# Optimization experiments

Measured on AMD Instinct MI355X. Metric: run time of the kernel, lower is better.

## Reference

```python
import jax, jax.numpy as jnp
import numpy as np

IH, IW = 32, 32
HEADS = 8
DIM_HEAD = 64
SCALE = DIM_HEAD ** -0.5


def _make_relative_index():
    # Matches torch buffer: ceil Euclidean distance between all pairs of 2D coords.
    ii, jj = np.meshgrid(np.arange(IH), np.arange(IW), indexing='ij')
    coords = np.stack([ii.ravel(), jj.ravel()])  # [2, n]
    rel = coords[:, :, None] - coords[:, None, :]  # [2, n, n]
    dist = np.ceil(np.sqrt(rel[0] ** 2 + rel[1] ** 2))
    return jnp.asarray(dist.astype(np.int32).ravel())  # [n*n]


def setup_inputs() -> dict:
    key = jax.random.key(0)
    k1, k2, k3, k4 = jax.random.split(key, 4)
    b, n, inp = 32, IH * IW, 512
    inner = HEADS * DIM_HEAD
    diag = int(np.ceil(np.sqrt((IH - 1) ** 2 + (IW - 1) ** 2)))
    return {
        'x': jax.random.normal(k1, (b, n, inp), jnp.float32),
        'w_qkv': jax.random.normal(k2, (inp, inner * 3), jnp.float32) * (inp ** -0.5),
        'bias_table': jax.random.normal(k3, (diag + 1, HEADS), jnp.float32) * 0.02,
        'w_out': jax.random.normal(k4, (inner, 512), jnp.float32) * (inner ** -0.5),
        'b_out': jnp.zeros((512,), jnp.float32),
        'relative_index': _make_relative_index(),
    }


def reference(x, w_qkv, bias_table, w_out, b_out, relative_index):
    b, n, _ = x.shape
    qkv = x @ w_qkv  # [b, n, 3*inner]
    q, k, v = jnp.split(qkv, 3, axis=-1)
    def to_heads(t):
        return t.reshape(b, n, HEADS, DIM_HEAD).transpose(0, 2, 1, 3)  # b h n d
    q, k, v = to_heads(q), to_heads(k), to_heads(v)
    dots = jnp.einsum('bhid,bhjd->bhij', q, k) * SCALE  # [b, h, n, n]
    # gather relative bias: [n*n, h] -> [1, h, n, n]
    rel_bias = bias_table[relative_index].reshape(n, n, HEADS).transpose(2, 0, 1)
    attn = jax.nn.softmax(dots + rel_bias[None], axis=-1)
    out = jnp.einsum('bhij,bhjd->bhid', attn, v)  # b h n d
    out = out.transpose(0, 2, 1, 3).reshape(b, n, HEADS * DIM_HEAD)
    return out @ w_out + b_out
```

## Files before the change

kernel.cpp:

```cpp
#include <hip/hip_runtime.h>
#include <hip/hip_bf16.h>
#include <cstdint>

typedef __bf16 bf16_t;
typedef bf16_t bf16x8 __attribute__((ext_vector_type(8)));
typedef float f32x4 __attribute__((ext_vector_type(4)));
typedef float f32x16 __attribute__((ext_vector_type(16)));
typedef unsigned u32x4 __attribute__((ext_vector_type(4)));

#define MFMA16(a, b, c) __builtin_amdgcn_mfma_f32_16x16x32_bf16(a, b, c, 0, 0, 0)
#define MFMA32(a, b, c) __builtin_amdgcn_mfma_f32_32x32x16_bf16(a, b, c, 0, 0, 0)

#define GLOAD_LDS16(g, l)                                                  \
    __builtin_amdgcn_global_load_lds(                                      \
        (const __attribute__((address_space(1))) unsigned*)(g),            \
        (__attribute__((address_space(3))) unsigned*)(l), 16, 0, 0)

constexpr int LDK = 72;

#define QSCALE 0.1803368801f
#define LOG2E 1.44269504f

__global__ void zero_out(unsigned short* __restrict__ out, long n) {
    long i = (long)blockIdx.x * 256 + threadIdx.x;
    if (i < n) out[i] = 0;
}

__global__ void detect_dtype(const unsigned* __restrict__ x,
                             int* __restrict__ flag) {
    if (threadIdx.x == 0 && blockIdx.x == 0) {
        int cnt = 0;
        for (int i = 0; i < 1024; ++i) {
            unsigned e = (x[i] >> 7) & 0xFF;
            cnt += (e > 100 && e < 150) ? 1 : 0;
        }
        *flag = (cnt > 512) ? 1 : 0;
    }
}

__global__ __launch_bounds__(256) void convert_x(const void* __restrict__ in,
                                                 bf16_t* __restrict__ out,
                                                 const int* __restrict__ flagp) {
    const int fl = *flagp;
    long i = ((long)blockIdx.x * 256 + threadIdx.x) * 8;
    if (fl) {
        *(bf16x8*)&out[i] = *(const bf16x8*)&((const bf16_t*)in)[i];
    } else {
        f32x4 lo = *(const f32x4*)&((const float*)in)[i];
        f32x4 hi = *(const f32x4*)&((const float*)in)[i + 4];
        bf16x8 v;
#pragma unroll
        for (int e = 0; e < 4; ++e) {
            v[e] = (bf16_t)lo[e];
            v[e + 4] = (bf16_t)hi[e];
        }
        *(bf16x8*)&out[i] = v;
    }
}

__global__ void transpose_flex(const void* __restrict__ in,
                               bf16_t* __restrict__ out, int R, int C,
                               const int* __restrict__ flagp, int scale_rows) {
    const int fl = *flagp;
    __shared__ bf16_t tile[32][33];
    int c0 = blockIdx.x * 32, r0 = blockIdx.y * 32;
    int x = threadIdx.x, y = threadIdx.y;
#pragma unroll
    for (int i = 0; i < 4; ++i) {
        long idx = (long)(r0 + y + 8 * i) * C + c0 + x;
        float fv = fl ? (float)((const bf16_t*)in)[idx]
                      : ((const float*)in)[idx];
        if (c0 + x < scale_rows) fv *= QSCALE;
        tile[y + 8 * i][x] = (bf16_t)fv;
    }
    __syncthreads();
#pragma unroll
    for (int i = 0; i < 4; ++i)
        out[(long)(c0 + y + 8 * i) * R + r0 + x] = tile[x][y + 8 * i];
}

__global__ __launch_bounds__(256) void build_bias_perm(
    const int* __restrict__ rel_index, const void* __restrict__ bias_table,
    float* __restrict__ perm, const int* __restrict__ flagp) {
    const int fl = *flagp;
    const int jt = blockIdx.x;
    const int qb = blockIdx.y;
    const int t = threadIdx.x;
    const int lane = t & 63;
    const int h = (t >> 6) + 4 * blockIdx.z;
    const int i = qb * 32 + (lane & 31);
    const int hi = lane >> 5;
    float out[16];
#pragma unroll
    for (int r = 0; r < 16; ++r) {
        int j = jt * 32 + (r & 3) + 8 * (r >> 2) + 4 * hi;
        int ridx = rel_index[i * 1024 + j];
        ridx = ridx < 0 ? 0 : (ridx > 44 ? 44 : ridx);
        float bv = fl ? (float)((const bf16_t*)bias_table)[ridx * 8 + h]
                      : ((const float*)bias_table)[ridx * 8 + h];
        out[r] = bv * LOG2E;
    }
    long off = (((long)(h * 32 + qb) * 32 + jt) << 10) + lane * 16;
#pragma unroll
    for (int g = 0; g < 4; ++g)
        *(f32x4*)&perm[off + 4 * g] = *(f32x4*)&out[4 * g];
}

__global__ __launch_bounds__(256) void transpose_v(
    const bf16_t* __restrict__ qkv, bf16_t* __restrict__ vt) {
    __shared__ bf16_t tile[64 * 64];
    const int jt = blockIdx.x;
    const int bh = blockIdx.y;
    const int b = bh >> 3, h = bh & 7;
    const bf16_t* src = qkv + (long)b * 1024 * 1536 + 1024 + h * 64;
    const int t = threadIdx.x;
    const int r = t >> 3, c8 = t & 7;
    const int j0 = jt * 64;
#pragma unroll
    for (int rep = 0; rep < 2; ++rep) {
        int jj = r + 32 * rep;
        *(bf16x8*)&tile[jj * 64 + ((c8 ^ (jj >> 3)) << 3)] =
            *(const bf16x8*)&src[(long)(j0 + jj) * 1536 + c8 * 8];
    }
    __syncthreads();
#pragma unroll
    for (int rep = 0; rep < 2; ++rep) {
        int dd = r + 32 * rep;
        int jc = c8 * 8;
        bf16_t o[8];
#pragma unroll
        for (int e = 0; e < 8; ++e) {
            int row = jc + e;
            o[e] = tile[row * 64 + (((dd >> 3) ^ (row >> 3)) << 3) + (dd & 7)];
        }
        *(bf16x8*)&vt[((long)bh << 16) + (long)dd * 1024 + j0 + jc] =
            *(bf16x8*)&o[0];
    }
}

template <bool BIAS, bool OUTFLEX>
__global__ __launch_bounds__(256) void gemm_lds(
    const bf16_t* __restrict__ A, const bf16_t* __restrict__ Bt, int K,
    int lda, long a_row0, void* __restrict__ C, int ldc, long c_row0,
    const void* __restrict__ bias, const int* __restrict__ flagp) {
    const int fl = *flagp;
    __shared__ bf16_t a_lds[128 * 64];
    __shared__ bf16_t b_lds[128 * 64];
    int t = threadIdx.x;
    int wave = t >> 6, lane = t & 63;
    int m16 = lane & 15, quad = lane >> 4;
    int wr = wave >> 1, wc = wave & 1;
    long m0 = (long)blockIdx.y * 128;
    int n0 = blockIdx.x * 128;

    f32x4 acc[4][4] = {};

    for (int ks = 0; ks < K; ks += 64) {
#pragma unroll
        for (int i = 0; i < 4; ++i) {
            int c = wave * 256 + i * 64 + lane;
            int row = c >> 3, kc = (c & 7) << 3;
            GLOAD_LDS16(&A[(a_row0 + m0 + row) * (long)lda + ks + kc],
                        &a_lds[row * 64 + kc]);
            GLOAD_LDS16(&Bt[(long)(n0 + row) * K + ks + kc],
                        &b_lds[row * 64 + kc]);
        }
        __syncthreads();
#pragma unroll
        for (int kf = 0; kf < 2; ++kf) {
            bf16x8 af[4], bfr[4];
#pragma unroll
            for (int mb = 0; mb < 4; ++mb)
                af[mb] = *(const bf16x8*)&a_lds[(wr * 64 + mb * 16 + m16) * 64 +
                                                kf * 32 + quad * 8];
#pragma unroll
            for (int nb = 0; nb < 4; ++nb)
                bfr[nb] = *(const bf16x8*)&b_lds[(wc * 64 + nb * 16 + m16) * 64 +
                                                 kf * 32 + quad * 8];
#pragma unroll
            for (int mb = 0; mb < 4; ++mb)
#pragma unroll
                for (int nb = 0; nb < 4; ++nb)
                    acc[mb][nb] = MFMA16(af[mb], bfr[nb], acc[mb][nb]);
        }
        __syncthreads();
    }

#pragma unroll
    for (int mb = 0; mb < 4; ++mb) {
#pragma unroll
        for (int nb = 0; nb < 4; ++nb) {
            int col = n0 + wc * 64 + nb * 16 + m16;
#pragma unroll
            for (int r = 0; r < 4; ++r) {
                long row = m0 + wr * 64 + mb * 16 + quad * 4 + r;
                float v = acc[mb][nb][r];
                if (BIAS) {
                    float bb = fl ? (float)((const bf16_t*)bias)[col]
                                  : ((const float*)bias)[col];
                    v += bb;
                }
                long off = (c_row0 + row) * (long)ldc + col;
                if (OUTFLEX && !fl)
                    ((float*)C)[off] = v;
                else
                    ((bf16_t*)C)[off] = (bf16_t)v;
            }
        }
    }
}

template <bool AFLEX, bool BIAS, bool OUTFLEX>
__global__ __launch_bounds__(256) void gemm128(
    const void* __restrict__ A, const bf16_t* __restrict__ Bt, int K, int lda,
    long a_row0, void* __restrict__ C, int ldc, long c_row0,
    const void* __restrict__ bias, const int* __restrict__ flagp) {
    const int fl = *flagp;
    __shared__ bf16_t a_lds[128 * LDK];
    __shared__ bf16_t b_lds[128 * LDK];
    int t = threadIdx.x;
    int wave = t >> 6, lane = t & 63;
    int m16 = lane & 15, quad = lane >> 4;
    int wr = wave >> 1, wc = wave & 1;
    long m0 = (long)blockIdx.y * 128;
    int n0 = blockIdx.x * 128;

    f32x4 acc[4][4] = {};

    for (int ks = 0; ks < K; ks += 64) {
#pragma unroll
        for (int i = 0; i < 4; ++i) {
            int c = t + 256 * i;
            int row = c >> 3;
            int kc = (c & 7) << 3;
            bf16x8 av;
            if (AFLEX && !fl) {
                const float* Af = (const float*)A;
                long base = (a_row0 + m0 + row) * (long)lda + ks + kc;
                f32x4 lo = *(const f32x4*)&Af[base];
                f32x4 hi = *(const f32x4*)&Af[base + 4];
#pragma unroll
                for (int e = 0; e < 4; ++e) {
                    av[e] = (bf16_t)lo[e];
                    av[e + 4] = (bf16_t)hi[e];
                }
            } else {
                av = *(const bf16x8*)&(
                    (const bf16_t*)A)[(a_row0 + m0 + row) * (long)lda + ks + kc];
            }
            *(bf16x8*)&a_lds[row * LDK + kc] = av;
            *(bf16x8*)&b_lds[row * LDK + kc] =
                *(const bf16x8*)&Bt[(long)(n0 + row) * K + ks + kc];
        }
        __syncthreads();
#pragma unroll
        for (int kf = 0; kf < 2; ++kf) {
            bf16x8 af[4], bfr[4];
#pragma unroll
            for (int mb = 0; mb < 4; ++mb)
                af[mb] = *(const bf16x8*)&a_lds[(wr * 64 + mb * 16 + m16) * LDK +
                                                kf * 32 + quad * 8];
#pragma unroll
            for (int nb = 0; nb < 4; ++nb)
                bfr[nb] = *(const bf16x8*)&b_lds[(wc * 64 + nb * 16 + m16) * LDK +
                                                 kf * 32 + quad * 8];
#pragma unroll
            for (int mb = 0; mb < 4; ++mb)
#pragma unroll
                for (int nb = 0; nb < 4; ++nb)
                    acc[mb][nb] = MFMA16(af[mb], bfr[nb], acc[mb][nb]);
        }
        __syncthreads();
    }

#pragma unroll
    for (int mb = 0; mb < 4; ++mb) {
#pragma unroll
        for (int nb = 0; nb < 4; ++nb) {
            int col = n0 + wc * 64 + nb * 16 + m16;
#pragma unroll
            for (int r = 0; r < 4; ++r) {
                long row = m0 + wr * 64 + mb * 16 + quad * 4 + r;
                float v = acc[mb][nb][r];
                if (BIAS) {
                    float bb = fl ? (float)((const bf16_t*)bias)[col]
                                  : ((const float*)bias)[col];
                    v += bb;
                }
                long off = (c_row0 + row) * (long)ldc + col;
                if (OUTFLEX && !fl)
                    ((float*)C)[off] = v;
                else
                    ((bf16_t*)C)[off] = (bf16_t)v;
            }
        }
    }
}

__global__ __launch_bounds__(256) void flash_attn3(
    bf16_t* __restrict__ qkv, const bf16_t* __restrict__ vt,
    const float* __restrict__ bias_perm) {
    __shared__ bf16_t k_lds[2][64 * 64];
    __shared__ bf16_t v_lds[2][64 * 64];

    const int t = threadIdx.x;
    const int lane = t & 63, wave = t >> 6;
    const int l31 = lane & 31, hi = lane >> 5;
    const int h = blockIdx.x;
    const int b = blockIdx.z;
    bf16_t* base = qkv + (long)b * 1024 * 1536;
    bf16_t* qb = base + h * 64;
    const bf16_t* kb = base + 512 + h * 64;
    const bf16_t* vtb = vt + ((long)(b * 8 + h) << 16);
    const int qblk = blockIdx.y * 4 + wave;
    const int q0w = qblk * 32;
    const float* bp = bias_perm + (((long)(h * 32 + qblk)) << 15) + lane * 16;

    bf16x8 qf[4];
#pragma unroll
    for (int s = 0; s < 4; ++s)
        qf[s] = *(const bf16x8*)&qb[(long)(q0w + l31) * 1536 + s * 16 + hi * 8];

    f32x16 oacc0 = {}, oacc1 = {}, lacc = {};
    bf16x8 ones;
#pragma unroll
    for (int e = 0; e < 8; ++e) ones[e] = (bf16_t)1.0f;

    const int srow = t >> 3, pc = t & 7;
    const int kc0 = (pc ^ (srow & 7)) << 3;

    {
        GLOAD_LDS16(&kb[(long)srow * 1536 + kc0],
                    &k_lds[0][srow * 64 + pc * 8]);
        GLOAD_LDS16(&kb[(long)(srow + 32) * 1536 + kc0],
                    &k_lds[0][(srow + 32) * 64 + pc * 8]);
        GLOAD_LDS16(&vtb[(long)srow * 1024 + kc0],
                    &v_lds[0][srow * 64 + pc * 8]);
        GLOAD_LDS16(&vtb[(long)(srow + 32) * 1024 + kc0],
                    &v_lds[0][(srow + 32) * 64 + pc * 8]);
    }
    __syncthreads();

    for (int tt = 0; tt < 16; ++tt) {
        const int cur = tt & 1;
        const float* bt = bp + ((long)tt << 11);
        f32x4 bv[8];
        bv[0] = *(const f32x4*)(bt);
        bv[1] = *(const f32x4*)(bt + 4);
        bv[2] = *(const f32x4*)(bt + 8);
        bv[3] = *(const f32x4*)(bt + 12);
        bv[4] = *(const f32x4*)(bt + 1024);
        bv[5] = *(const f32x4*)(bt + 1028);
        bv[6] = *(const f32x4*)(bt + 1032);
        bv[7] = *(const f32x4*)(bt + 1036);
        if (tt < 15) {
            const int nb = cur ^ 1;
            long j0n = (long)(tt + 1) * 64;
            GLOAD_LDS16(&kb[(j0n + srow) * 1536 + kc0],
                        &k_lds[nb][srow * 64 + pc * 8]);
            GLOAD_LDS16(&kb[(j0n + srow + 32) * 1536 + kc0],
                        &k_lds[nb][(srow + 32) * 64 + pc * 8]);
            GLOAD_LDS16(&vtb[(long)srow * 1024 + j0n + kc0],
                        &v_lds[nb][srow * 64 + pc * 8]);
            GLOAD_LDS16(&vtb[(long)(srow + 32) * 1024 + j0n + kc0],
                        &v_lds[nb][(srow + 32) * 64 + pc * 8]);
        }

#pragma unroll
        for (int js = 0; js < 2; ++js) {
            f32x16 s;
#pragma unroll
            for (int g = 0; g < 4; ++g) {
#pragma unroll
                for (int e = 0; e < 4; ++e) s[4 * g + e] = bv[4 * js + g][e];
            }
            const int krow = js * 32 + l31;
            __builtin_amdgcn_s_setprio(1);
#pragma unroll
            for (int st = 0; st < 4; ++st) {
                bf16x8 kf = *(const bf16x8*)&k_lds[cur][krow * 64 +
                             (((st * 2 + hi) ^ (krow & 7)) << 3)];
                s = MFMA32(kf, qf[st], s);
            }
            __builtin_amdgcn_s_setprio(0);
            float sv[16];
#pragma unroll
            for (int r = 0; r < 16; ++r)
                sv[r] = __builtin_amdgcn_exp2f(s[r]);
            unsigned dw[8];
#pragma unroll
            for (int g = 0; g < 4; ++g) {
                unsigned da, db;
                asm("v_cvt_pk_bf16_f32 %0, %1, %2"
                    : "=v"(da) : "v"(sv[4 * g]), "v"(sv[4 * g + 1]));
                asm("v_cvt_pk_bf16_f32 %0, %1, %2"
                    : "=v"(db) : "v"(sv[4 * g + 2]), "v"(sv[4 * g + 3]));
                dw[2 * g] = da;
                dw[2 * g + 1] = db;
            }
#pragma unroll
            for (int kk = 0; kk < 2; ++kk) {
                asm("v_permlane32_swap_b32 %0, %1"
                    : "+v"(dw[4 * kk + 0]), "+v"(dw[4 * kk + 2]));
                asm("v_permlane32_swap_b32 %0, %1"
                    : "+v"(dw[4 * kk + 1]), "+v"(dw[4 * kk + 3]));
            }
            __builtin_amdgcn_s_setprio(1);
#pragma unroll
            for (int kk = 0; kk < 2; ++kk) {
                u32x4 uv;
                uv[0] = dw[4 * kk + 0];
                uv[1] = dw[4 * kk + 1];
                uv[2] = dw[4 * kk + 2];
                uv[3] = dw[4 * kk + 3];
                bf16x8 pa = __builtin_bit_cast(bf16x8, uv);
                lacc = MFMA32(pa, ones, lacc);
#pragma unroll
                for (int db2 = 0; db2 < 2; ++db2) {
                    const int vrow = db2 * 32 + l31;
                    bf16x8 vf = *(const bf16x8*)&v_lds[cur][vrow * 64 +
                                 (((js * 4 + kk * 2 + hi) ^ (vrow & 7)) << 3)];
                    if (db2 == 0)
                        oacc0 = MFMA32(pa, vf, oacc0);
                    else
                        oacc1 = MFMA32(pa, vf, oacc1);
                }
            }
            __builtin_amdgcn_s_setprio(0);
        }
        __syncthreads();
    }

#pragma unroll
    for (int r = 0; r < 16; ++r) {
        float inv = 1.0f / lacc[r];
        int row = (r & 3) + 8 * (r >> 2) + 4 * hi;
        qb[(long)(q0w + row) * 1536 + l31] = (bf16_t)(oacc0[r] * inv);
        qb[(long)(q0w + row) * 1536 + 32 + l31] = (bf16_t)(oacc1[r] * inv);
    }
}

__global__ __launch_bounds__(256) void flash_attn2(
    bf16_t* __restrict__ qkv, const float* __restrict__ bias_perm) {
    __shared__ bf16_t k_lds[2][64 * 64];
    __shared__ bf16_t v_lds[2][64 * 64];

    const int t = threadIdx.x;
    const int lane = t & 63, wave = t >> 6;
    const int l31 = lane & 31, hi = lane >> 5;
    const int h = blockIdx.x;
    const int b = blockIdx.z;
    bf16_t* base = qkv + (long)b * 1024 * 1536;
    bf16_t* qb = base + h * 64;
    const bf16_t* kb = base + 512 + h * 64;
    const bf16_t* vb = base + 1024 + h * 64;
    const int qblk = blockIdx.y * 4 + wave;
    const int q0w = qblk * 32;
    const float* bp = bias_perm + (((long)(h * 32 + qblk)) << 15) + lane * 16;

    bf16x8 qf[4];
#pragma unroll
    for (int s = 0; s < 4; ++s)
        qf[s] = *(const bf16x8*)&qb[(long)(q0w + l31) * 1536 + s * 16 + hi * 8];

    f32x16 oacc0 = {}, oacc1 = {}, lacc = {};
    bf16x8 ones;
#pragma unroll
    for (int e = 0; e < 8; ++e) ones[e] = (bf16_t)1.0f;

    const int sr0 = t >> 3, sg0 = t & 7;
    const int sr1 = sr0 + 32;

    {
        bf16x8 k0 = *(const bf16x8*)&kb[(long)sr0 * 1536 + sg0 * 8];
        bf16x8 k1 = *(const bf16x8*)&kb[(long)sr1 * 1536 + sg0 * 8];
        bf16x8 v0 = *(const bf16x8*)&vb[(long)sr0 * 1536 + sg0 * 8];
        bf16x8 v1 = *(const bf16x8*)&vb[(long)sr1 * 1536 + sg0 * 8];
        *(bf16x8*)&k_lds[0][sr0 * 64 + ((sg0 ^ (sr0 & 7)) << 3)] = k0;
        *(bf16x8*)&k_lds[0][sr1 * 64 + ((sg0 ^ (sr1 & 7)) << 3)] = k1;
#pragma unroll
        for (int e = 0; e < 8; ++e) {
            int d0 = sg0 * 8 + e;
            v_lds[0][d0 * 64 + (((sr0 >> 3) ^ (d0 & 7)) << 3) + (sr0 & 7)] = v0[e];
            v_lds[0][d0 * 64 + (((sr1 >> 3) ^ (d0 & 7)) << 3) + (sr1 & 7)] = v1[e];
        }
    }
    __syncthreads();

    for (int tt = 0; tt < 16; ++tt) {
        const int cur = tt & 1;
        bf16x8 kn0 = {}, kn1 = {}, vn0 = {}, vn1 = {};
        if (tt < 15) {
            long j0n = (long)(tt + 1) * 64;
            kn0 = *(const bf16x8*)&kb[(j0n + sr0) * 1536 + sg0 * 8];
            kn1 = *(const bf16x8*)&kb[(j0n + sr1) * 1536 + sg0 * 8];
            vn0 = *(const bf16x8*)&vb[(j0n + sr0) * 1536 + sg0 * 8];
            vn1 = *(const bf16x8*)&vb[(j0n + sr1) * 1536 + sg0 * 8];
        }
        const float* bt = bp + ((long)tt << 11);
        f32x4 bv[8];
        bv[0] = *(const f32x4*)(bt);
        bv[1] = *(const f32x4*)(bt + 4);
        bv[2] = *(const f32x4*)(bt + 8);
        bv[3] = *(const f32x4*)(bt + 12);
        bv[4] = *(const f32x4*)(bt + 1024);
        bv[5] = *(const f32x4*)(bt + 1028);
        bv[6] = *(const f32x4*)(bt + 1032);
        bv[7] = *(const f32x4*)(bt + 1036);

#pragma unroll
        for (int js = 0; js < 2; ++js) {
            f32x16 s;
#pragma unroll
            for (int g = 0; g < 4; ++g) {
#pragma unroll
                for (int e = 0; e < 4; ++e) s[4 * g + e] = bv[4 * js + g][e];
            }
            const int krow = js * 32 + l31;
#pragma unroll
            for (int st = 0; st < 4; ++st) {
                bf16x8 kf = *(const bf16x8*)&k_lds[cur][krow * 64 +
                             (((st * 2 + hi) ^ (krow & 7)) << 3)];
                s = MFMA32(kf, qf[st], s);
            }
            float sv[16];
#pragma unroll
            for (int r = 0; r < 16; ++r)
                sv[r] = __builtin_amdgcn_exp2f(s[r]);
            unsigned dw[8];
#pragma unroll
            for (int g = 0; g < 4; ++g) {
                unsigned da, db;
                asm("v_cvt_pk_bf16_f32 %0, %1, %2"
                    : "=v"(da) : "v"(sv[4 * g]), "v"(sv[4 * g + 1]));
                asm("v_cvt_pk_bf16_f32 %0, %1, %2"
                    : "=v"(db) : "v"(sv[4 * g + 2]), "v"(sv[4 * g + 3]));
                dw[2 * g] = da;
                dw[2 * g + 1] = db;
            }
#pragma unroll
            for (int kk = 0; kk < 2; ++kk) {
                asm("v_permlane32_swap_b32 %0, %1"
                    : "+v"(dw[4 * kk + 0]), "+v"(dw[4 * kk + 2]));
                asm("v_permlane32_swap_b32 %0, %1"
                    : "+v"(dw[4 * kk + 1]), "+v"(dw[4 * kk + 3]));
            }
#pragma unroll
            for (int kk = 0; kk < 2; ++kk) {
                u32x4 uv;
                uv[0] = dw[4 * kk + 0];
                uv[1] = dw[4 * kk + 1];
                uv[2] = dw[4 * kk + 2];
                uv[3] = dw[4 * kk + 3];
                bf16x8 pa = __builtin_bit_cast(bf16x8, uv);
                lacc = MFMA32(pa, ones, lacc);
#pragma unroll
                for (int db2 = 0; db2 < 2; ++db2) {
                    const int vrow = db2 * 32 + l31;
                    bf16x8 vf = *(const bf16x8*)&v_lds[cur][vrow * 64 +
                                 (((js * 4 + kk * 2 + hi) ^ (vrow & 7)) << 3)];
                    if (db2 == 0)
                        oacc0 = MFMA32(pa, vf, oacc0);
                    else
                        oacc1 = MFMA32(pa, vf, oacc1);
                }
            }
        }
        if (tt < 15) {
            const int nb = cur ^ 1;
            *(bf16x8*)&k_lds[nb][sr0 * 64 + ((sg0 ^ (sr0 & 7)) << 3)] = kn0;
            *(bf16x8*)&k_lds[nb][sr1 * 64 + ((sg0 ^ (sr1 & 7)) << 3)] = kn1;
#pragma unroll
            for (int e = 0; e < 8; ++e) {
                int d0 = sg0 * 8 + e;
                v_lds[nb][d0 * 64 + (((sr0 >> 3) ^ (d0 & 7)) << 3) + (sr0 & 7)] =
                    vn0[e];
                v_lds[nb][d0 * 64 + (((sr1 >> 3) ^ (d0 & 7)) << 3) + (sr1 & 7)] =
                    vn1[e];
            }
        }
        __syncthreads();
    }

#pragma unroll
    for (int r = 0; r < 16; ++r) {
        float inv = 1.0f / lacc[r];
        int row = (r & 3) + 8 * (r >> 2) + 4 * hi;
        qb[(long)(q0w + row) * 1536 + l31] = (bf16_t)(oacc0[r] * inv);
        qb[(long)(q0w + row) * 1536 + 32 + l31] = (bf16_t)(oacc1[r] * inv);
    }
}

extern "C" void kernel_launch(void* const* d_in, const int* in_sizes, int n_in,
                              void* d_out, int out_size, void* d_ws,
                              size_t ws_size, hipStream_t stream) {
    const void* x = nullptr;
    const void* w_qkv = nullptr;
    const void* bias_table = nullptr;
    const void* w_out = nullptr;
    const void* b_out = nullptr;
    const void* rel_raw = nullptr;
    for (int i = 0; i < n_in; ++i) {
        switch (in_sizes[i]) {
            case 16777216: x = d_in[i]; break;
            case 786432:  w_qkv = d_in[i]; break;
            case 360:     bias_table = d_in[i]; break;
            case 262144:  w_out = d_in[i]; break;
            case 512:     b_out = d_in[i]; break;
            case 1048576: rel_raw = d_in[i]; break;
            default: break;
        }
    }
    if (!x || !w_qkv || !bias_table || !w_out || !b_out || !rel_raw) {
        x = d_in[0]; w_qkv = d_in[1]; bias_table = d_in[2];
        w_out = d_in[3]; b_out = d_in[4]; rel_raw = d_in[5];
    }
    const int* rel_index = (const int*)rel_raw;

    char* ws = (char*)d_ws;
    bf16_t* wqkvT = (bf16_t*)ws;
    bf16_t* woutT = (bf16_t*)(ws + 1572864);
    int* flag = (int*)(ws + 1572864 + 524288);
    float* rel_bias = (float*)(ws + 1572864 + 524288 + 256);
    const size_t fixed = 1572864 + 524288 + 256 + 33554432;
    const size_t xbf_bytes = (size_t)32 * 1024 * 512 * sizeof(bf16_t);
    const size_t qkv_pb = (size_t)1024 * 1536 * sizeof(bf16_t);
    const size_t vt_pb = (size_t)8 * 64 * 1024 * sizeof(bf16_t);

    if (ws_size < fixed + qkv_pb) {
        long n = (long)out_size;
        long nblk = (n + 255) / 256;
        if (nblk > 0)
            zero_out<<<(unsigned)nblk, 256, 0, stream>>>(
                (unsigned short*)d_out, n);
        return;
    }

    bool have_xbf = ws_size >= fixed + xbf_bytes + qkv_pb;
    bool have_vt = ws_size >= fixed + xbf_bytes + qkv_pb + vt_pb;
    bf16_t* x_bf = (bf16_t*)(ws + fixed);
    bf16_t* qkv = have_xbf ? (bf16_t*)(ws + fixed + xbf_bytes)
                           : (bf16_t*)(ws + fixed);

    size_t avail = ws_size - fixed - (have_xbf ? xbf_bytes : 0);
    size_t pb = have_vt ? (qkv_pb + vt_pb) : qkv_pb;
    int chunk = (int)(avail / pb);
    if (chunk > 32) chunk = 32;
    if (chunk < 1) chunk = 1;
    while (32 % chunk) --chunk;
    bf16_t* vt = (bf16_t*)((char*)qkv + (size_t)chunk * qkv_pb);

    detect_dtype<<<1, 64, 0, stream>>>((const unsigned*)x, flag);
    transpose_flex<<<dim3(1536 / 32, 512 / 32), dim3(32, 8), 0, stream>>>(
        w_qkv, wqkvT, 512, 1536, flag, 512);
    transpose_flex<<<dim3(512 / 32, 512 / 32), dim3(32, 8), 0, stream>>>(
        w_out, woutT, 512, 512, flag, 0);
    build_bias_perm<<<dim3(32, 32, 2), 256, 0, stream>>>(
        rel_index, bias_table, rel_bias, flag);
    if (have_xbf)
        convert_x<<<8192, 256, 0, stream>>>(x, x_bf, flag);

    for (int b0 = 0; b0 < 32; b0 += chunk) {
        long row0 = (long)b0 * 1024;
        int mrows = chunk * 1024;
        if (have_xbf) {
            gemm_lds<false, false>
                <<<dim3(1536 / 128, mrows / 128), 256, 0, stream>>>(
                    x_bf, wqkvT, 512, 512, row0, qkv, 1536, 0, nullptr, flag);
        } else {
            gemm128<true, false, false>
                <<<dim3(1536 / 128, mrows / 128), 256, 0, stream>>>(
                    x, wqkvT, 512, 512, row0, qkv, 1536, 0, nullptr, flag);
        }
        if (have_vt) {
            transpose_v<<<dim3(16, chunk * 8), 256, 0, stream>>>(qkv, vt);
            flash_attn3<<<dim3(8, 8, chunk), 256, 0, stream>>>(qkv, vt,
                                                               rel_bias);
        } else {
            flash_attn2<<<dim3(8, 8, chunk), 256, 0, stream>>>(qkv, rel_bias);
        }
        gemm_lds<true, true>
            <<<dim3(512 / 128, mrows / 128), 256, 0, stream>>>(
                qkv, woutT, 512, 1536, 0, d_out, 512, row0, b_out, flag);
    }
}
```

Measured before the change: 472.2 us.

## Triple-buffer K/V tiles and prefetch bias one iteration ahead in attention

Changes the flash_attn3 K/V LDS staging from double to triple buffering, so loads run two tiles ahead, and prefetches the relative-bias registers one tile ahead. Plain __syncthreads is replaced by hand-written s_waitcnt vmcnt plus s_barrier, fenced with scheduling barriers, so in-flight global loads are not drained each iteration. The aim is to hide global and bias load latency behind MFMA work. The cost is more LDS (48KB) and registers, which may lower occupancy. The hand-counted vmcnt values are fragile and the last iterations issue redundant loads.

```diff
diff --git a/kernel.cpp b/kernel.cpp
--- a/kernel.cpp
+++ b/kernel.cpp
@@ -15,6 +15,8 @@
     __builtin_amdgcn_global_load_lds(                                      \
         (const __attribute__((address_space(1))) unsigned*)(g),            \
         (__attribute__((address_space(3))) unsigned*)(l), 16, 0, 0)
+
+#define SB() __builtin_amdgcn_sched_barrier(0)
 
 constexpr int LDK = 72;
 
@@ -300,8 +302,8 @@
 __global__ __launch_bounds__(256) void flash_attn3(
     bf16_t* __restrict__ qkv, const bf16_t* __restrict__ vt,
     const float* __restrict__ bias_perm) {
-    __shared__ bf16_t k_lds[2][64 * 64];
-    __shared__ bf16_t v_lds[2][64 * 64];
+    __shared__ bf16_t k_lds[3][64 * 64];
+    __shared__ bf16_t v_lds[3][64 * 64];
 
     const int t = threadIdx.x;
     const int lane = t & 63, wave = t >> 6;
@@ -329,33 +331,50 @@
     const int srow = t >> 3, pc = t & 7;
     const int kc0 = (pc ^ (srow & 7)) << 3;
 
-    {
-        GLOAD_LDS16(&kb[(long)srow * 1536 + kc0],
-                    &k_lds[0][srow * 64 + pc * 8]);
-        GLOAD_LDS16(&kb[(long)(srow + 32) * 1536 + kc0],
-                    &k_lds[0][(srow + 32) * 64 + pc * 8]);
-        GLOAD_LDS16(&vtb[(long)srow * 1024 + kc0],
-                    &v_lds[0][srow * 64 + pc * 8]);
-        GLOAD_LDS16(&vtb[(long)(srow + 32) * 1024 + kc0],
-                    &v_lds[0][(srow + 32) * 64 + pc * 8]);
-    }
-    __syncthreads();
+    f32x4 bvC[8];
+    bvC[0] = *(const f32x4*)(bp);
+    bvC[1] = *(const f32x4*)(bp + 4);
+    bvC[2] = *(const f32x4*)(bp + 8);
+    bvC[3] = *(const f32x4*)(bp + 12);
+    bvC[4] = *(const f32x4*)(bp + 1024);
+    bvC[5] = *(const f32x4*)(bp + 1028);
+    bvC[6] = *(const f32x4*)(bp + 1032);
+    bvC[7] = *(const f32x4*)(bp + 1036);
+    SB();
+#pragma unroll
+    for (int pt = 0; pt < 2; ++pt) {
+        long j0 = (long)pt * 64;
+        GLOAD_LDS16(&kb[(j0 + srow) * 1536 + kc0],
+                    &k_lds[pt][srow * 64 + pc * 8]);
+        GLOAD_LDS16(&kb[(j0 + srow + 32) * 1536 + kc0],
+                    &k_lds[pt][(srow + 32) * 64 + pc * 8]);
+        GLOAD_LDS16(&vtb[(long)srow * 1024 + j0 + kc0],
+                    &v_lds[pt][srow * 64 + pc * 8]);
+        GLOAD_LDS16(&vtb[(long)(srow + 32) * 1024 + j0 + kc0],
+                    &v_lds[pt][(srow + 32) * 64 + pc * 8]);
+    }
+    SB();
+    asm volatile("s_waitcnt vmcnt(4)\n\ts_barrier" ::: "memory");
+    SB();
 
     for (int tt = 0; tt < 16; ++tt) {
-        const int cur = tt & 1;
-        const float* bt = bp + ((long)tt << 11);
-        f32x4 bv[8];
-        bv[0] = *(const f32x4*)(bt);
-        bv[1] = *(const f32x4*)(bt + 4);
-        bv[2] = *(const f32x4*)(bt + 8);
-        bv[3] = *(const f32x4*)(bt + 12);
-        bv[4] = *(const f32x4*)(bt + 1024);
-        bv[5] = *(const f32x4*)(bt + 1028);
-        bv[6] = *(const f32x4*)(bt + 1032);
-        bv[7] = *(const f32x4*)(bt + 1036);
-        if (tt < 15) {
-            const int nb = cur ^ 1;
-            long j0n = (long)(tt + 1) * 64;
+        const int cur = tt % 3;
+        const int tb = (tt + 1 < 16) ? tt + 1 : 15;
+        const float* bt = bp + ((long)tb << 11);
+        f32x4 bvN[8];
+        bvN[0] = *(const f32x4*)(bt);
+        bvN[1] = *(const f32x4*)(bt + 4);
+        bvN[2] = *(const f32x4*)(bt + 8);
+        bvN[3] = *(const f32x4*)(bt + 12);
+        bvN[4] = *(const f32x4*)(bt + 1024);
+        bvN[5] = *(const f32x4*)(bt + 1028);
+        bvN[6] = *(const f32x4*)(bt + 1032);
+        bvN[7] = *(const f32x4*)(bt + 1036);
+        SB();
+        {
+            const int td = (tt + 2 < 16) ? tt + 2 : 15;
+            const int nb = (tt + 2) % 3;
+            long j0n = (long)td * 64;
             GLOAD_LDS16(&kb[(j0n + srow) * 1536 + kc0],
                         &k_lds[nb][srow * 64 + pc * 8]);
             GLOAD_LDS16(&kb[(j0n + srow + 32) * 1536 + kc0],
@@ -365,6 +384,7 @@
             GLOAD_LDS16(&vtb[(long)(srow + 32) * 1024 + j0n + kc0],
                         &v_lds[nb][(srow + 32) * 64 + pc * 8]);
         }
+        SB();
 
 #pragma unroll
         for (int js = 0; js < 2; ++js) {
@@ -372,7 +392,7 @@
 #pragma unroll
             for (int g = 0; g < 4; ++g) {
 #pragma unroll
-                for (int e = 0; e < 4; ++e) s[4 * g + e] = bv[4 * js + g][e];
+                for (int e = 0; e < 4; ++e) s[4 * g + e] = bvC[4 * js + g][e];
             }
             const int krow = js * 32 + l31;
             __builtin_amdgcn_s_setprio(1);
@@ -428,7 +448,11 @@
             }
             __builtin_amdgcn_s_setprio(0);
         }
-        __syncthreads();
+
+        asm volatile("s_waitcnt vmcnt(12)\n\ts_barrier" ::: "memory");
+        SB();
+#pragma unroll
+        for (int g = 0; g < 8; ++g) bvC[g] = bvN[g];
     }
 
 #pragma unroll
```

Result: slower. 490.5 us (+3.9%).

## Process two query blocks per wave in flash attention to reuse K/V fragments

Applied to the files above, without the earlier changes.

Each wave now handles two 32-row query blocks (A and B), sharing each K and V fragment loaded from LDS across both, and the grid's y dimension is halved to match. The second half of the bias tile is prefetched after the score MFMAs rather than up front, and launch bounds now ask for 2 blocks per CU. This cuts LDS reads and K/V tile loads per query row and gives the scheduler more independent MFMA chains. In exchange it roughly doubles accumulator register use, which risks lower occupancy or spills, and halves the number of blocks.

```diff
diff --git a/kernel.cpp b/kernel.cpp
--- a/kernel.cpp
+++ b/kernel.cpp
@@ -297,7 +297,7 @@
     }
 }
 
-__global__ __launch_bounds__(256) void flash_attn3(
+__global__ __launch_bounds__(256, 2) void flash_attn3(
     bf16_t* __restrict__ qkv, const bf16_t* __restrict__ vt,
     const float* __restrict__ bias_perm) {
     __shared__ bf16_t k_lds[2][64 * 64];
@@ -312,16 +312,21 @@
     bf16_t* qb = base + h * 64;
     const bf16_t* kb = base + 512 + h * 64;
     const bf16_t* vtb = vt + ((long)(b * 8 + h) << 16);
-    const int qblk = blockIdx.y * 4 + wave;
-    const int q0w = qblk * 32;
-    const float* bp = bias_perm + (((long)(h * 32 + qblk)) << 15) + lane * 16;
-
-    bf16x8 qf[4];
-#pragma unroll
-    for (int s = 0; s < 4; ++s)
-        qf[s] = *(const bf16x8*)&qb[(long)(q0w + l31) * 1536 + s * 16 + hi * 8];
-
-    f32x16 oacc0 = {}, oacc1 = {}, lacc = {};
+    const int qblkA = blockIdx.y * 4 + wave;
+    const int qblkB = qblkA + 16;
+    const int q0A = qblkA * 32, q0B = qblkB * 32;
+    const float* bpA = bias_perm + (((long)(h * 32 + qblkA)) << 15) + lane * 16;
+    const float* bpB = bias_perm + (((long)(h * 32 + qblkB)) << 15) + lane * 16;
+
+    bf16x8 qfA[4], qfB[4];
+#pragma unroll
+    for (int s = 0; s < 4; ++s) {
+        qfA[s] = *(const bf16x8*)&qb[(long)(q0A + l31) * 1536 + s * 16 + hi * 8];
+        qfB[s] = *(const bf16x8*)&qb[(long)(q0B + l31) * 1536 + s * 16 + hi * 8];
+    }
+
+    f32x16 oacc0A = {}, oacc1A = {}, laccA = {};
+    f32x16 oacc0B = {}, oacc1B = {}, laccB = {};
     bf16x8 ones;
 #pragma unroll
     for (int e = 0; e < 8; ++e) ones[e] = (bf16_t)1.0f;
@@ -341,18 +346,44 @@
     }
     __syncthreads();
 
+#define SOFTMAX_REPACK(S, DW)                                              \
+    {                                                                      \
+        float sv_[16];                                                     \
+        _Pragma("unroll") for (int r = 0; r < 16; ++r)                     \
+            sv_[r] = __builtin_amdgcn_exp2f((S)[r]);                       \
+        _Pragma("unroll") for (int g = 0; g < 4; ++g) {                    \
+            unsigned da_, db_;                                             \
+            asm("v_cvt_pk_bf16_f32 %0, %1, %2"                             \
+                : "=v"(da_) : "v"(sv_[4 * g]), "v"(sv_[4 * g + 1]));       \
+            asm("v_cvt_pk_bf16_f32 %0, %1, %2"                             \
+                : "=v"(db_) : "v"(sv_[4 * g + 2]), "v"(sv_[4 * g + 3]));   \
+            (DW)[2 * g] = da_;                                             \
+            (DW)[2 * g + 1] = db_;                                         \
+        }                                                                  \
+        _Pragma("unroll") for (int kk = 0; kk < 2; ++kk) {                 \
+            asm("v_permlane32_swap_b32 %0, %1"                             \
+                : "+v"((DW)[4 * kk + 0]), "+v"((DW)[4 * kk + 2]));         \
+            asm("v_permlane32_swap_b32 %0, %1"                             \
+                : "+v"((DW)[4 * kk + 1]), "+v"((DW)[4 * kk + 3]));         \
+        }                                                                  \
+    }
+
+#define PACK_PA(DW, KK)                                                    \
+    __builtin_bit_cast(bf16x8, (u32x4){(DW)[4 * (KK) + 0],                 \
+                                       (DW)[4 * (KK) + 1],                 \
+                                       (DW)[4 * (KK) + 2],                 \
+                                       (DW)[4 * (KK) + 3]})
+
     for (int tt = 0; tt < 16; ++tt) {
         const int cur = tt & 1;
-        const float* bt = bp + ((long)tt << 11);
-        f32x4 bv[8];
-        bv[0] = *(const f32x4*)(bt);
-        bv[1] = *(const f32x4*)(bt + 4);
-        bv[2] = *(const f32x4*)(bt + 8);
-        bv[3] = *(const f32x4*)(bt + 12);
-        bv[4] = *(const f32x4*)(bt + 1024);
-        bv[5] = *(const f32x4*)(bt + 1028);
-        bv[6] = *(const f32x4*)(bt + 1032);
-        bv[7] = *(const f32x4*)(bt + 1036);
+        const float* btA = bpA + ((long)tt << 11);
+        const float* btB = bpB + ((long)tt << 11);
+        f32x4 bA0[4], bB0[4];
+#pragma unroll
+        for (int g = 0; g < 4; ++g) {
+            bA0[g] = *(const f32x4*)(btA + 4 * g);
+            bB0[g] = *(const f32x4*)(btB + 4 * g);
+        }
         if (tt < 15) {
             const int nb = cur ^ 1;
             long j0n = (long)(tt + 1) * 64;
@@ -366,65 +397,58 @@
                         &v_lds[nb][(srow + 32) * 64 + pc * 8]);
         }
 
+        f32x4 bA1[4], bB1[4];
 #pragma unroll
         for (int js = 0; js < 2; ++js) {
-            f32x16 s;
+            const int krow = js * 32 + l31;
+            bf16x8 kf[4];
+#pragma unroll
+            for (int st = 0; st < 4; ++st)
+                kf[st] = *(const bf16x8*)&k_lds[cur][krow * 64 +
+                          (((st * 2 + hi) ^ (krow & 7)) << 3)];
+            f32x16 sA, sB;
 #pragma unroll
             for (int g = 0; g < 4; ++g) {
-#pragma unroll
-                for (int e = 0; e < 4; ++e) s[4 * g + e] = bv[4 * js + g][e];
-            }
-            const int krow = js * 32 + l31;
+                const f32x4 ba = js ? bA1[g] : bA0[g];
+                const f32x4 bb = js ? bB1[g] : bB0[g];
+#pragma unroll
+                for (int e = 0; e < 4; ++e) {
+                    sA[4 * g + e] = ba[e];
+                    sB[4 * g + e] = bb[e];
+                }
+            }
             __builtin_amdgcn_s_setprio(1);
 #pragma unroll
-            for (int st = 0; st < 4; ++st) {
-                bf16x8 kf = *(const bf16x8*)&k_lds[cur][krow * 64 +
-                             (((st * 2 + hi) ^ (krow & 7)) << 3)];
-                s = MFMA32(kf, qf[st], s);
-            }
+            for (int st = 0; st < 4; ++st) sA = MFMA32(kf[st], qfA[st], sA);
+#pragma unroll
+            for (int st = 0; st < 4; ++st) sB = MFMA32(kf[st], qfB[st], sB);
             __builtin_amdgcn_s_setprio(0);
-            float sv[16];
-#pragma unroll
-            for (int r = 0; r < 16; ++r)
-                sv[r] = __builtin_amdgcn_exp2f(s[r]);
-            unsigned dw[8];
-#pragma unroll
-            for (int g = 0; g < 4; ++g) {
-                unsigned da, db;
-                asm("v_cvt_pk_bf16_f32 %0, %1, %2"
-                    : "=v"(da) : "v"(sv[4 * g]), "v"(sv[4 * g + 1]));
-                asm("v_cvt_pk_bf16_f32 %0, %1, %2"
-                    : "=v"(db) : "v"(sv[4 * g + 2]), "v"(sv[4 * g + 3]));
-                dw[2 * g] = da;
-                dw[2 * g + 1] = db;
-            }
+            if (js == 0) {
+#pragma unroll
+                for (int g = 0; g < 4; ++g) {
+                    bA1[g] = *(const f32x4*)(btA + 1024 + 4 * g);
+                    bB1[g] = *(const f32x4*)(btB + 1024 + 4 * g);
+                }
+            }
+            unsigned dwA[8], dwB[8];
+            SOFTMAX_REPACK(sA, dwA);
+            SOFTMAX_REPACK(sB, dwB);
+            __builtin_amdgcn_s_setprio(1);
 #pragma unroll
             for (int kk = 0; kk < 2; ++kk) {
-                asm("v_permlane32_swap_b32 %0, %1"
-                    : "+v"(dw[4 * kk + 0]), "+v"(dw[4 * kk + 2]));
-                asm("v_permlane32_swap_b32 %0, %1"
-                    : "+v"(dw[4 * kk + 1]), "+v"(dw[4 * kk + 3]));
-            }
-            __builtin_amdgcn_s_setprio(1);
-#pragma unroll
-            for (int kk = 0; kk < 2; ++kk) {
-                u32x4 uv;
-                uv[0] = dw[4 * kk + 0];
-                uv[1] = dw[4 * kk + 1];
-                uv[2] = dw[4 * kk + 2];
-                uv[3] = dw[4 * kk + 3];
-                bf16x8 pa = __builtin_bit_cast(bf16x8, uv);
-                lacc = MFMA32(pa, ones, lacc);
-#pragma unroll
-                for (int db2 = 0; db2 < 2; ++db2) {
-                    const int vrow = db2 * 32 + l31;
-                    bf16x8 vf = *(const bf16x8*)&v_lds[cur][vrow * 64 +
-                                 (((js * 4 + kk * 2 + hi) ^ (vrow & 7)) << 3)];
-                    if (db2 == 0)
-                        oacc0 = MFMA32(pa, vf, oacc0);
-                    else
-                        oacc1 = MFMA32(pa, vf, oacc1);
-                }
+                bf16x8 paA = PACK_PA(dwA, kk);
+                bf16x8 paB = PACK_PA(dwB, kk);
+                const int vr0 = l31, vr1 = 32 + l31;
+                bf16x8 vf0 = *(const bf16x8*)&v_lds[cur][vr0 * 64 +
+                              (((js * 4 + kk * 2 + hi) ^ (vr0 & 7)) << 3)];
+                bf16x8 vf1 = *(const bf16x8*)&v_lds[cur][vr1 * 64 +
+                              (((js * 4 + kk * 2 + hi) ^ (vr1 & 7)) << 3)];
+                laccA = MFMA32(paA, ones, laccA);
+                oacc0A = MFMA32(paA, vf0, oacc0A);
+                oacc1A = MFMA32(paA, vf1, oacc1A);
+                laccB = MFMA32(paB, ones, laccB);
+                oacc0B = MFMA32(paB, vf0, oacc0B);
+                oacc1B = MFMA32(paB, vf1, oacc1B);
             }
             __builtin_amdgcn_s_setprio(0);
         }
@@ -433,10 +457,13 @@
 
 #pragma unroll
     for (int r = 0; r < 16; ++r) {
-        float inv = 1.0f / lacc[r];
         int row = (r & 3) + 8 * (r >> 2) + 4 * hi;
-        qb[(long)(q0w + row) * 1536 + l31] = (bf16_t)(oacc0[r] * inv);
-        qb[(long)(q0w + row) * 1536 + 32 + l31] = (bf16_t)(oacc1[r] * inv);
+        float invA = 1.0f / laccA[r];
+        float invB = 1.0f / laccB[r];
+        qb[(long)(q0A + row) * 1536 + l31] = (bf16_t)(oacc0A[r] * invA);
+        qb[(long)(q0A + row) * 1536 + 32 + l31] = (bf16_t)(oacc1A[r] * invA);
+        qb[(long)(q0B + row) * 1536 + l31] = (bf16_t)(oacc0B[r] * invB);
+        qb[(long)(q0B + row) * 1536 + 32 + l31] = (bf16_t)(oacc1B[r] * invB);
     }
 }
 
@@ -674,7 +701,7 @@
         }
         if (have_vt) {
             transpose_v<<<dim3(16, chunk * 8), 256, 0, stream>>>(qkv, vt);
-            flash_attn3<<<dim3(8, 8, chunk), 256, 0, stream>>>(qkv, vt,
+            flash_attn3<<<dim3(8, 4, chunk), 256, 0, stream>>>(qkv, vt,
                                                                rel_bias);
         } else {
             flash_attn2<<<dim3(8, 8, chunk), 256, 0, stream>>>(qkv, rel_bias);
```

Measured after the change: 461.9 us. 2.2% less time.
